# Performance work log

Measured on AMD Instinct MI355X. Metric: run time of the kernel, lower is better.

The kernel has to match this reference:

```python
import jax, jax.numpy as jnp
import numpy as np
import math

B, N, M, C, H = 4, 2048, 2048, 512, 4
D_V = C // H          # 128, used for scale and value head dim
D_QK = 2 * C // H     # 256, q/k head dim due to seq-axis split of the 2*dim qkv output
SCALE = D_V ** -0.5
EPS = 1e-12           # F.normalize eps


def _l2norm(t):
    n = jnp.linalg.norm(t, axis=-1, keepdims=True)
    return t / jnp.maximum(n, EPS)


def setup_inputs() -> dict:
    key = jax.random.key(0)
    k1, k2, k3, k4 = jax.random.split(key, 4)
    x = jax.random.normal(k1, (B, N, C), dtype=jnp.float32)
    context = jax.random.normal(k2, (B, M, C), dtype=jnp.float32)
    W_qkv = jax.random.normal(k3, (2 * C, C), dtype=jnp.float32) * 0.02  # torch Linear weight [out,in]
    W_proj = jax.random.normal(k4, (C, C), dtype=jnp.float32) * 0.02
    radius = jnp.ones((H,), dtype=jnp.float32) * math.sqrt(D_V)
    return {"x": x, "context": context, "W_qkv": W_qkv, "W_proj": W_proj, "radius": radius}


def reference(x, context, W_qkv, W_proj, radius):
    # qkv(cat([x, context], dim=1)) then split along sequence: q from x rows, k from context rows
    q = jnp.einsum('bnc,oc->bno', x, W_qkv)        # [B,N,2C]
    k = jnp.einsum('bmc,oc->bmo', context, W_qkv)  # [B,M,2C]
    q = q.reshape(B, N, H, D_QK).transpose(0, 2, 1, 3)       # [B,H,N,256]
    k = k.reshape(B, M, H, D_QK).transpose(0, 2, 1, 3)       # [B,H,M,256]
    v = context.reshape(B, M, H, D_V).transpose(0, 2, 1, 3)  # [B,H,M,128]
    r = radius[None, :, None, None]
    q = _l2norm(q) * r
    k = _l2norm(k) * r
    attn = jnp.einsum('bhnd,bhmd->bhnm', q, k) * SCALE
    attn = jax.nn.softmax(attn, axis=-1)
    out = jnp.einsum('bhnm,bhmd->bhnd', attn, v)
    out = out.transpose(0, 2, 1, 3).reshape(B, N, C)
    return jnp.einsum('bnc,oc->bno', out, W_proj)
```

## Files before the change

kernel.cpp:

```cpp
#include <hip/hip_runtime.h>
#include <hip/hip_bf16.h>
#include <stdint.h>

#define SCALE_F 0.08838834764831845f
#define LOG2E_F 1.4426950408889634f

typedef __attribute__((ext_vector_type(8))) short short8;
typedef __attribute__((ext_vector_type(4))) float f32x4;
typedef __attribute__((ext_vector_type(16))) float f32x16;
typedef __attribute__((ext_vector_type(2))) unsigned int uint2v;

__device__ __forceinline__ void g2l16(const void* g, void* l) {
  __builtin_amdgcn_global_load_lds(
      (const __attribute__((address_space(1))) void*)g,
      (__attribute__((address_space(3))) void*)l, 16, 0, 0);
}

__device__ __forceinline__ unsigned pkbf(float a, float b) {
  union { __hip_bfloat16 h[2]; unsigned u; } o;
  o.h[0] = __float2bfloat16(a); o.h[1] = __float2bfloat16(b);
  return o.u;
}

__device__ __forceinline__ float fexp2(float x) {
#if __has_builtin(__builtin_amdgcn_exp2f)
  return __builtin_amdgcn_exp2f(x);
#else
  float r; asm("v_exp_f32 %0, %1" : "=v"(r) : "v"(x)); return r;
#endif
}

__global__ __launch_bounds__(256) void convert_all(
    const float* __restrict__ x, const float* __restrict__ wqkv,
    const float* __restrict__ wproj,
    __hip_bfloat16* __restrict__ ab, __hip_bfloat16* __restrict__ wb,
    __hip_bfloat16* __restrict__ wpb)
{
  size_t qi = (size_t)blockIdx.x * 256 + threadIdx.x;
  const float* src; __hip_bfloat16* dst; size_t off;
  if (qi < 1048576)      { src = x;     dst = ab;  off = qi; }
  else if (qi < 1179648) { src = wqkv;  dst = wb;  off = qi - 1048576; }
  else                   { src = wproj; dst = wpb; off = qi - 1179648; }
  float4 v = ((const float4*)src)[off];
  union { __hip_bfloat16 h4[4]; uint2 u; } o;
  o.h4[0] = __float2bfloat16(v.x); o.h4[1] = __float2bfloat16(v.y);
  o.h4[2] = __float2bfloat16(v.z); o.h4[3] = __float2bfloat16(v.w);
  ((uint2*)dst)[off] = o.u;
}

__global__ __launch_bounds__(256) void transpose_v(
    const float* __restrict__ ctx, __hip_bfloat16* __restrict__ vt,
    __hip_bfloat16* __restrict__ abctx)
{
  __shared__ float tile[128][33];
  const int bid = blockIdx.x;
  const int mt = bid & 63;
  const int bh = bid >> 6;
  const int h = bh & 3, b = bh >> 2;
  const int tid = threadIdx.x;
  for (int i = 0; i < 16; ++i) {
    int idx = i * 256 + tid;
    int mm = idx >> 7, d = idx & 127;
    tile[d][mm] = ctx[((size_t)b * 2048 + mt * 32 + mm) * 512 + h * 128 + d];
  }
  __syncthreads();
  for (int i = 0; i < 16; ++i) {
    int idx = i * 256 + tid;
    int d = idx >> 5, mm = idx & 31;
    vt[((size_t)bh * 128 + d) * 2048 + mt * 32 + mm] = __float2bfloat16(tile[d][mm]);
  }
  for (int i = 0; i < 16; ++i) {
    int idx = i * 256 + tid;
    int mm = idx >> 7, d = idx & 127;
    abctx[((size_t)b * 2048 + mt * 32 + mm) * 512 + h * 128 + d] =
        __float2bfloat16(tile[d][mm]);
  }
}

__global__ __launch_bounds__(256) void gemm_qkv(
    const __hip_bfloat16* __restrict__ A,
    const __hip_bfloat16* __restrict__ Bw,
    const float* __restrict__ radius,
    __hip_bfloat16* __restrict__ qn, __hip_bfloat16* __restrict__ kn)
{
  __shared__ __hip_bfloat16 sAB[320 * 32];
  __shared__ float sNorm[4][64];
  __hip_bfloat16* sA = sAB;
  __hip_bfloat16* sB = sAB + 64 * 32;
  const int tid = threadIdx.x;
  const int wave = tid >> 6, lane = tid & 63;
  const int ln = lane & 15, q4 = lane >> 4;
  const int ro = blockIdx.x >> 2;
  const int co = blockIdx.x & 3;
  const __hip_bfloat16* Ab = A + (size_t)ro * 64 * 512;
  const __hip_bfloat16* Bb = Bw + (size_t)co * 256 * 512;
  const int row0 = tid >> 2, p0 = tid & 3;
  f32x4 acc[4][4] = {};
  for (int k0 = 0; k0 < 512; k0 += 32) {
    g2l16(Ab + (size_t)row0 * 512 + k0 + p0 * 8, (char*)sA + tid * 16);
#pragma unroll
    for (int i = 0; i < 4; ++i)
      g2l16(Bb + (size_t)(i * 64 + row0) * 512 + k0 + p0 * 8,
            (char*)sB + (i * 256 + tid) * 16);
    __syncthreads();
    short8 af[4], bfr[4];
#pragma unroll
    for (int mi = 0; mi < 4; ++mi)
      af[mi] = *(const short8*)(sA + (mi * 16 + ln) * 32 + q4 * 8);
#pragma unroll
    for (int ni = 0; ni < 4; ++ni)
      bfr[ni] = *(const short8*)(sB + (wave * 64 + ni * 16 + ln) * 32 + q4 * 8);
#pragma unroll
    for (int mi = 0; mi < 4; ++mi)
#pragma unroll
      for (int ni = 0; ni < 4; ++ni)
        acc[mi][ni] = __builtin_amdgcn_mfma_f32_16x16x32_bf16(af[mi], bfr[ni], acc[mi][ni], 0, 0, 0);
    __syncthreads();
  }
  const float rad = radius[co];
  const int grow0 = ro * 64;
  const bool isq = grow0 < 8192;
  const int rl = isq ? grow0 : grow0 - 8192;
  const float qfac = isq ? rad * rad * SCALE_F * LOG2E_F : 1.0f;
#pragma unroll
  for (int mi = 0; mi < 4; ++mi)
#pragma unroll
    for (int r = 0; r < 4; ++r) {
      float ss = acc[mi][0][r] * acc[mi][0][r] + acc[mi][1][r] * acc[mi][1][r]
               + acc[mi][2][r] * acc[mi][2][r] + acc[mi][3][r] * acc[mi][3][r];
      ss += __shfl_xor(ss, 1); ss += __shfl_xor(ss, 2);
      ss += __shfl_xor(ss, 4); ss += __shfl_xor(ss, 8);
      if (ln == 0) sNorm[wave][mi * 16 + q4 * 4 + r] = ss;
    }
  __syncthreads();
  float scl[4][4];
#pragma unroll
  for (int mi = 0; mi < 4; ++mi)
#pragma unroll
    for (int r = 0; r < 4; ++r) {
      int row = mi * 16 + q4 * 4 + r;
      float tot = sNorm[0][row] + sNorm[1][row] + sNorm[2][row] + sNorm[3][row];
      scl[mi][r] = qfac / fmaxf(sqrtf(tot), 1e-12f);
    }
  __hip_bfloat16* dstT = (isq ? qn : kn) +
      ((size_t)((rl >> 11) * 4 + co) * 2048 + (rl & 2047)) * 256;
  __hip_bfloat16* sE = sAB;
#pragma unroll
  for (int c = 0; c < 2; ++c) {
#pragma unroll
    for (int mi2 = 0; mi2 < 2; ++mi2) {
      int mi = c * 2 + mi2;
#pragma unroll
      for (int r = 0; r < 4; ++r) {
        int lr = mi2 * 16 + q4 * 4 + r;
#pragma unroll
        for (int ni = 0; ni < 4; ++ni)
          sE[lr * 264 + wave * 64 + ni * 16 + ln] =
              __float2bfloat16(acc[mi][ni][r] * scl[mi][r]);
      }
    }
    __syncthreads();
#pragma unroll
    for (int p = 0; p < 4; ++p) {
      int idx = p * 256 + tid;
      int rr = idx >> 5, c8 = idx & 31;
      short8 v = *(const short8*)(sE + rr * 264 + c8 * 8);
      *(short8*)(dstT + (size_t)(c * 32 + rr) * 256 + c8 * 8) = v;
    }
    __syncthreads();
  }
}

__global__ __launch_bounds__(256) void gemm_nt(
    const __hip_bfloat16* __restrict__ A, const __hip_bfloat16* __restrict__ B,
    float* __restrict__ C, int O, int K, int tiles_o)
{
  __shared__ __hip_bfloat16 sA[128 * 32];
  __shared__ __hip_bfloat16 sB[128 * 32];
  const int tid = threadIdx.x;
  const int wave = tid >> 6, lane = tid & 63;
  const int ln = lane & 15, q = lane >> 4;
  const int br = (blockIdx.x / tiles_o) * 128;
  const int bo = (blockIdx.x % tiles_o) * 128;
  const int wr = (wave >> 1) * 64, wc = (wave & 1) * 64;
  const __hip_bfloat16* Ab = A + (size_t)br * K;
  const __hip_bfloat16* Bb = B + (size_t)bo * K;
  const int row0 = tid >> 2, p0 = tid & 3;
  f32x4 acc[4][4] = {};
  for (int k0 = 0; k0 < K; k0 += 32) {
    for (int i = 0; i < 2; ++i) {
      int row = i * 64 + row0;
      g2l16(Ab + (size_t)row * K + k0 + p0 * 8, (char*)sA + (i * 256 + tid) * 16);
      g2l16(Bb + (size_t)row * K + k0 + p0 * 8, (char*)sB + (i * 256 + tid) * 16);
    }
    __syncthreads();
    short8 af[4], bfr[4];
    for (int mi = 0; mi < 4; ++mi)
      af[mi] = *(const short8*)(sA + (wr + mi * 16 + ln) * 32 + q * 8);
    for (int ni = 0; ni < 4; ++ni)
      bfr[ni] = *(const short8*)(sB + (wc + ni * 16 + ln) * 32 + q * 8);
    for (int mi = 0; mi < 4; ++mi)
      for (int ni = 0; ni < 4; ++ni)
        acc[mi][ni] = __builtin_amdgcn_mfma_f32_16x16x32_bf16(af[mi], bfr[ni], acc[mi][ni], 0, 0, 0);
    __syncthreads();
  }
  for (int mi = 0; mi < 4; ++mi)
    for (int ni = 0; ni < 4; ++ni) {
      int rg = br + wr + mi * 16 + q * 4;
      int cg = bo + wc + ni * 16 + ln;
      for (int r = 0; r < 4; ++r)
        C[(size_t)(rg + r) * O + cg] = acc[mi][ni][r];
    }
}

__global__ __launch_bounds__(256, 2) void attn(
    const __hip_bfloat16* __restrict__ qn,
    const __hip_bfloat16* __restrict__ kn,
    const __hip_bfloat16* __restrict__ vt,
    float* __restrict__ Op,
    float* __restrict__ den)
{
  __shared__ __hip_bfloat16 sK[2][32 * 256];
  __shared__ __hip_bfloat16 sV[2][128 * 32];
  const int tid = threadIdx.x, wave = tid >> 6, lane = tid & 63;
  const int m32 = lane & 31, hi = lane >> 5;
  const int i = blockIdx.x;
  const int bh = (i & 7) + 8 * ((i >> 3) & 1);
  const int half = (i >> 4) & 1;
  const int nt = i >> 5;
  const int mbase = half * 1024;
  const __hip_bfloat16* Q = qn + ((size_t)bh * 2048 + nt * 128 + wave * 32) * 256;
  const __hip_bfloat16* Kp = kn + (size_t)bh * 2048 * 256;
  const __hip_bfloat16* Vp = vt + (size_t)bh * 128 * 2048;

  short8 qf[16];
  for (int kk = 0; kk < 16; ++kk)
    qf[kk] = *(const short8*)(Q + m32 * 256 + kk * 16 + hi * 8);

  f32x16 oacc[4];
  for (int v = 0; v < 4; ++v)
    for (int j = 0; j < 16; ++j) oacc[v][j] = 0.f;
  float denom = 0.f;

  for (int t = 0; t < 4; ++t) {
    int D = t * 256 + tid, row = D >> 5, cc = D & 31;
    g2l16(Kp + (size_t)(mbase + row) * 256 + ((cc ^ (row & 7)) << 3),
          (char*)sK[0] + D * 16);
  }
  for (int t = 0; t < 2; ++t) {
    int D = t * 256 + tid, rd = D >> 2, cc = D & 3;
    g2l16(Vp + (size_t)rd * 2048 + mbase + ((cc ^ ((rd >> 1) & 3)) << 3),
          (char*)sV[0] + D * 16);
  }
  __syncthreads();

  for (int it = 0; it < 32; ++it) {
    const int cur = it & 1, nxt = cur ^ 1;
    if (it + 1 < 32) {
      const int m1 = mbase + (it + 1) * 32;
      for (int t = 0; t < 4; ++t) {
        int D = t * 256 + tid, row = D >> 5, cc = D & 31;
        g2l16(Kp + (size_t)(m1 + row) * 256 + ((cc ^ (row & 7)) << 3),
              (char*)sK[nxt] + D * 16);
      }
      for (int t = 0; t < 2; ++t) {
        int D = t * 256 + tid, rd = D >> 2, cc = D & 3;
        g2l16(Vp + (size_t)rd * 2048 + m1 + ((cc ^ ((rd >> 1) & 3)) << 3),
              (char*)sV[nxt] + D * 16);
      }
    }
    const __hip_bfloat16* sKc = sK[cur];
    f32x16 sa, sb;
    for (int j = 0; j < 16; ++j) { sa[j] = 0.f; sb[j] = 0.f; }
#pragma unroll
    for (int kk = 0; kk < 8; ++kk) {
      int ca = kk * 2 + hi, cb = (kk + 8) * 2 + hi;
      short8 kfa = *(const short8*)(sKc + m32 * 256 + ((ca ^ (m32 & 7)) << 3));
      short8 kfb = *(const short8*)(sKc + m32 * 256 + ((cb ^ (m32 & 7)) << 3));
      sa = __builtin_amdgcn_mfma_f32_32x32x16_bf16(kfa, qf[kk], sa, 0, 0, 0);
      sb = __builtin_amdgcn_mfma_f32_32x32x16_bf16(kfb, qf[kk + 8], sb, 0, 0, 0);
    }
    union { unsigned u[4]; short8 s; } ua, ub;
    {
      float e0, e1, e2, e3;
      unsigned u0, u1, u2, u3;
      e0 = fexp2(sa[0] + sb[0]); e1 = fexp2(sa[1] + sb[1]);
      e2 = fexp2(sa[2] + sb[2]); e3 = fexp2(sa[3] + sb[3]);
      denom += (e0 + e1) + (e2 + e3);
      u0 = pkbf(e0, e1); u1 = pkbf(e2, e3);
      e0 = fexp2(sa[4] + sb[4]); e1 = fexp2(sa[5] + sb[5]);
      e2 = fexp2(sa[6] + sb[6]); e3 = fexp2(sa[7] + sb[7]);
      denom += (e0 + e1) + (e2 + e3);
      u2 = pkbf(e0, e1); u3 = pkbf(e2, e3);
      uint2v s0 = __builtin_amdgcn_permlane32_swap(u0, u2, false, false);
      uint2v s1 = __builtin_amdgcn_permlane32_swap(u1, u3, false, false);
      ua.u[0] = s0.x; ua.u[1] = s1.x; ua.u[2] = s0.y; ua.u[3] = s1.y;
      e0 = fexp2(sa[8] + sb[8]);   e1 = fexp2(sa[9] + sb[9]);
      e2 = fexp2(sa[10] + sb[10]); e3 = fexp2(sa[11] + sb[11]);
      denom += (e0 + e1) + (e2 + e3);
      u0 = pkbf(e0, e1); u1 = pkbf(e2, e3);
      e0 = fexp2(sa[12] + sb[12]); e1 = fexp2(sa[13] + sb[13]);
      e2 = fexp2(sa[14] + sb[14]); e3 = fexp2(sa[15] + sb[15]);
      denom += (e0 + e1) + (e2 + e3);
      u2 = pkbf(e0, e1); u3 = pkbf(e2, e3);
      uint2v s2 = __builtin_amdgcn_permlane32_swap(u0, u2, false, false);
      uint2v s3 = __builtin_amdgcn_permlane32_swap(u1, u3, false, false);
      ub.u[0] = s2.x; ub.u[1] = s3.x; ub.u[2] = s2.y; ub.u[3] = s3.y;
    }
    const __hip_bfloat16* sVc = sV[cur];
#pragma unroll
    for (int kc = 0; kc < 2; ++kc) {
      short8 pf = kc ? ub.s : ua.s;
#pragma unroll
      for (int vi = 0; vi < 4; ++vi) {
        int rd = vi * 32 + m32;
        int c = kc * 2 + hi;
        short8 vf = *(const short8*)(sVc + rd * 32 + ((c ^ ((rd >> 1) & 3)) << 3));
        oacc[vi] = __builtin_amdgcn_mfma_f32_32x32x16_bf16(vf, pf, oacc[vi], 0, 0, 0);
      }
    }
    __syncthreads();
  }

  float dfull = denom + __shfl_xor(denom, 32);
  float* Opb = Op + (size_t)(half * 16 + bh) * 2048 * 128;
  float* denb = den + (size_t)(half * 16 + bh) * 2048;
  const int rbase = nt * 128 + wave * 32;
  if (hi == 0) denb[rbase + m32] = dfull;
  float* sc_ = (float*)(&sK[0][0]) + wave * 1056;
#pragma unroll
  for (int vi = 0; vi < 4; ++vi) {
#pragma unroll
    for (int reg = 0; reg < 16; ++reg) {
      int dL = (reg & 3) + 8 * (reg >> 2) + 4 * hi;
      sc_[m32 * 33 + dL] = oacc[vi][reg];
    }
    asm volatile("s_waitcnt lgkmcnt(0)" ::: "memory");
#pragma unroll
    for (int qq = 0; qq < 16; ++qq) {
      int qr = qq * 2 + hi;
      Opb[(size_t)(rbase + qr) * 128 + vi * 32 + m32] = sc_[qr * 33 + m32];
    }
    asm volatile("s_waitcnt lgkmcnt(0)" ::: "memory");
  }
}

__global__ __launch_bounds__(256) void combine(
    const float* __restrict__ Op, const float* __restrict__ den,
    __hip_bfloat16* __restrict__ ob)
{
  int qi = blockIdx.x * 256 + threadIdx.x;
  int r = qi >> 5;
  int dq = qi & 31;
  int bh = r >> 11, n = r & 2047, b = bh >> 2, h = bh & 3;
  float4 o0 = ((const float4*)Op)[qi];
  float4 o1 = ((const float4*)(Op + 4194304))[qi];
  float inv = 1.0f / (den[r] + den[32768 + r]);
  union { __hip_bfloat16 h4[4]; uint2 u; } o;
  o.h4[0] = __float2bfloat16((o0.x + o1.x) * inv);
  o.h4[1] = __float2bfloat16((o0.y + o1.y) * inv);
  o.h4[2] = __float2bfloat16((o0.z + o1.z) * inv);
  o.h4[3] = __float2bfloat16((o0.w + o1.w) * inv);
  *(uint2*)&ob[((size_t)b * 2048 + n) * 512 + h * 128 + dq * 4] = o.u;
}

extern "C" void kernel_launch(void* const* d_in, const int* in_sizes, int n_in,
                              void* d_out, int out_size, void* d_ws, size_t ws_size,
                              hipStream_t stream) {
  const float* x      = (const float*)d_in[0];
  const float* ctx    = (const float*)d_in[1];
  const float* wqkv   = (const float*)d_in[2];
  const float* wproj  = (const float*)d_in[3];
  const float* radius = (const float*)d_in[4];
  char* ws = (char*)d_ws;
  __hip_bfloat16* ab  = (__hip_bfloat16*)(ws);
  __hip_bfloat16* wb  = (__hip_bfloat16*)(ws + 16777216);
  __hip_bfloat16* wpb = (__hip_bfloat16*)(ws + 17825792);
  float*          Op  = (float*)(ws + 18350080);
  float*          den = (float*)(ws + 18350080 + 33554432);
  __hip_bfloat16* qn  = (__hip_bfloat16*)(ws + 85458944);
  __hip_bfloat16* kn  = (__hip_bfloat16*)(ws + 102236160);
  __hip_bfloat16* vt  = (__hip_bfloat16*)(ws + 119013376);
  __hip_bfloat16* ob  = (__hip_bfloat16*)(ws + 127401984);
  float* out = (float*)d_out;

  convert_all<<<4864, 256, 0, stream>>>(x, wqkv, wproj, ab, wb, wpb);
  transpose_v<<<1024, 256, 0, stream>>>(ctx, vt, ab + 4194304);
  gemm_qkv<<<1024, 256, 0, stream>>>(ab, wb, radius, qn, kn);
  attn<<<512, 256, 0, stream>>>(qn, kn, vt, Op, den);
  combine<<<4096, 256, 0, stream>>>(Op, den, ob);
  gemm_nt<<<256, 256, 0, stream>>>(ob, wpb, out, 512, 512, 4);
}
```

Baseline: 214.3 us.

## Software-pipeline QK and softmax-PV across KV tiles with triple buffering

The attention loop is restructured so each iteration issues the QK^T MFMAs for the next KV tile before the exp/pack and PV MFMAs of the current tile. A third LDS buffer holds the extra tile in flight, and the waits become explicit vmcnt waits plus barriers. This lets exp and permlane work overlap with matrix ops, at the cost of more registers for a second score set and more LDS per block. The output projection GEMM is specialized to 128x64 tiles with 512 blocks for better CU coverage.

Measured after the change: 242.8 us. +13.3%, slower.

```diff
diff --git a/kernel.cpp b/kernel.cpp
--- a/kernel.cpp
+++ b/kernel.cpp
@@ -171,46 +171,128 @@
   }
 }
 
-__global__ __launch_bounds__(256) void gemm_nt(
-    const __hip_bfloat16* __restrict__ A, const __hip_bfloat16* __restrict__ B,
-    float* __restrict__ C, int O, int K, int tiles_o)
+__global__ __launch_bounds__(256) void gemm_proj(
+    const __hip_bfloat16* __restrict__ A,
+    const __hip_bfloat16* __restrict__ B,
+    float* __restrict__ C)
 {
   __shared__ __hip_bfloat16 sA[128 * 32];
-  __shared__ __hip_bfloat16 sB[128 * 32];
+  __shared__ __hip_bfloat16 sB[64 * 32];
   const int tid = threadIdx.x;
   const int wave = tid >> 6, lane = tid & 63;
   const int ln = lane & 15, q = lane >> 4;
-  const int br = (blockIdx.x / tiles_o) * 128;
-  const int bo = (blockIdx.x % tiles_o) * 128;
-  const int wr = (wave >> 1) * 64, wc = (wave & 1) * 64;
-  const __hip_bfloat16* Ab = A + (size_t)br * K;
-  const __hip_bfloat16* Bb = B + (size_t)bo * K;
+  const int br = (blockIdx.x >> 3) * 128;
+  const int bo = (blockIdx.x & 7) * 64;
+  const int wr = (wave >> 1) * 64, wc = (wave & 1) * 32;
   const int row0 = tid >> 2, p0 = tid & 3;
-  f32x4 acc[4][4] = {};
-  for (int k0 = 0; k0 < K; k0 += 32) {
-    for (int i = 0; i < 2; ++i) {
-      int row = i * 64 + row0;
-      g2l16(Ab + (size_t)row * K + k0 + p0 * 8, (char*)sA + (i * 256 + tid) * 16);
-      g2l16(Bb + (size_t)row * K + k0 + p0 * 8, (char*)sB + (i * 256 + tid) * 16);
-    }
-    __syncthreads();
-    short8 af[4], bfr[4];
+  f32x4 acc[4][2] = {};
+  for (int k0 = 0; k0 < 512; k0 += 32) {
+    g2l16(A + (size_t)(br + row0) * 512 + k0 + p0 * 8, (char*)sA + tid * 16);
+    g2l16(A + (size_t)(br + 64 + row0) * 512 + k0 + p0 * 8,
+          (char*)sA + (256 + tid) * 16);
+    g2l16(B + (size_t)(bo + row0) * 512 + k0 + p0 * 8, (char*)sB + tid * 16);
+    __syncthreads();
+    short8 af[4], bfr[2];
+#pragma unroll
     for (int mi = 0; mi < 4; ++mi)
       af[mi] = *(const short8*)(sA + (wr + mi * 16 + ln) * 32 + q * 8);
-    for (int ni = 0; ni < 4; ++ni)
+#pragma unroll
+    for (int ni = 0; ni < 2; ++ni)
       bfr[ni] = *(const short8*)(sB + (wc + ni * 16 + ln) * 32 + q * 8);
+#pragma unroll
     for (int mi = 0; mi < 4; ++mi)
-      for (int ni = 0; ni < 4; ++ni)
+#pragma unroll
+      for (int ni = 0; ni < 2; ++ni)
         acc[mi][ni] = __builtin_amdgcn_mfma_f32_16x16x32_bf16(af[mi], bfr[ni], acc[mi][ni], 0, 0, 0);
     __syncthreads();
   }
+#pragma unroll
   for (int mi = 0; mi < 4; ++mi)
-    for (int ni = 0; ni < 4; ++ni) {
+#pragma unroll
+    for (int ni = 0; ni < 2; ++ni) {
       int rg = br + wr + mi * 16 + q * 4;
       int cg = bo + wc + ni * 16 + ln;
+#pragma unroll
       for (int r = 0; r < 4; ++r)
-        C[(size_t)(rg + r) * O + cg] = acc[mi][ni][r];
-    }
+        C[(size_t)(rg + r) * 512 + cg] = acc[mi][ni][r];
+    }
+}
+
+__device__ __forceinline__ void stage_kv(
+    const __hip_bfloat16* __restrict__ Kp, const __hip_bfloat16* __restrict__ Vp,
+    int mrow, __hip_bfloat16* dK, __hip_bfloat16* dV, int tid)
+{
+#pragma unroll
+  for (int t = 0; t < 4; ++t) {
+    int D = t * 256 + tid, row = D >> 5, cc = D & 31;
+    g2l16(Kp + (size_t)(mrow + row) * 256 + ((cc ^ (row & 7)) << 3),
+          (char*)dK + D * 16);
+  }
+#pragma unroll
+  for (int t = 0; t < 2; ++t) {
+    int D = t * 256 + tid, rd = D >> 2, cc = D & 3;
+    g2l16(Vp + (size_t)rd * 2048 + mrow + ((cc ^ ((rd >> 1) & 3)) << 3),
+          (char*)dV + D * 16);
+  }
+}
+
+__device__ __forceinline__ void qk_step(
+    const __hip_bfloat16* __restrict__ sKc, const short8* qf,
+    int m32, int hi, f32x16& sa, f32x16& sb)
+{
+  for (int j = 0; j < 16; ++j) { sa[j] = 0.f; sb[j] = 0.f; }
+#pragma unroll
+  for (int kk = 0; kk < 8; ++kk) {
+    int ca = kk * 2 + hi, cb = (kk + 8) * 2 + hi;
+    short8 kfa = *(const short8*)(sKc + m32 * 256 + ((ca ^ (m32 & 7)) << 3));
+    short8 kfb = *(const short8*)(sKc + m32 * 256 + ((cb ^ (m32 & 7)) << 3));
+    sa = __builtin_amdgcn_mfma_f32_32x32x16_bf16(kfa, qf[kk], sa, 0, 0, 0);
+    sb = __builtin_amdgcn_mfma_f32_32x32x16_bf16(kfb, qf[kk + 8], sb, 0, 0, 0);
+  }
+}
+
+__device__ __forceinline__ void smpv_step(
+    const f32x16& sa, const f32x16& sb, const __hip_bfloat16* __restrict__ sVc,
+    int m32, int hi, f32x16* oacc, float& denom)
+{
+  union { unsigned u[4]; short8 s; } ua, ub;
+  {
+    float e0, e1, e2, e3;
+    unsigned u0, u1, u2, u3;
+    e0 = fexp2(sa[0] + sb[0]); e1 = fexp2(sa[1] + sb[1]);
+    e2 = fexp2(sa[2] + sb[2]); e3 = fexp2(sa[3] + sb[3]);
+    denom += (e0 + e1) + (e2 + e3);
+    u0 = pkbf(e0, e1); u1 = pkbf(e2, e3);
+    e0 = fexp2(sa[4] + sb[4]); e1 = fexp2(sa[5] + sb[5]);
+    e2 = fexp2(sa[6] + sb[6]); e3 = fexp2(sa[7] + sb[7]);
+    denom += (e0 + e1) + (e2 + e3);
+    u2 = pkbf(e0, e1); u3 = pkbf(e2, e3);
+    uint2v s0 = __builtin_amdgcn_permlane32_swap(u0, u2, false, false);
+    uint2v s1 = __builtin_amdgcn_permlane32_swap(u1, u3, false, false);
+    ua.u[0] = s0.x; ua.u[1] = s1.x; ua.u[2] = s0.y; ua.u[3] = s1.y;
+    e0 = fexp2(sa[8] + sb[8]);   e1 = fexp2(sa[9] + sb[9]);
+    e2 = fexp2(sa[10] + sb[10]); e3 = fexp2(sa[11] + sb[11]);
+    denom += (e0 + e1) + (e2 + e3);
+    u0 = pkbf(e0, e1); u1 = pkbf(e2, e3);
+    e0 = fexp2(sa[12] + sb[12]); e1 = fexp2(sa[13] + sb[13]);
+    e2 = fexp2(sa[14] + sb[14]); e3 = fexp2(sa[15] + sb[15]);
+    denom += (e0 + e1) + (e2 + e3);
+    u2 = pkbf(e0, e1); u3 = pkbf(e2, e3);
+    uint2v s2 = __builtin_amdgcn_permlane32_swap(u0, u2, false, false);
+    uint2v s3 = __builtin_amdgcn_permlane32_swap(u1, u3, false, false);
+    ub.u[0] = s2.x; ub.u[1] = s3.x; ub.u[2] = s2.y; ub.u[3] = s3.y;
+  }
+#pragma unroll
+  for (int kc = 0; kc < 2; ++kc) {
+    short8 pf = kc ? ub.s : ua.s;
+#pragma unroll
+    for (int vi = 0; vi < 4; ++vi) {
+      int rd = vi * 32 + m32;
+      int c = kc * 2 + hi;
+      short8 vf = *(const short8*)(sVc + rd * 32 + ((c ^ ((rd >> 1) & 3)) << 3));
+      oacc[vi] = __builtin_amdgcn_mfma_f32_32x32x16_bf16(vf, pf, oacc[vi], 0, 0, 0);
+    }
+  }
 }
 
 __global__ __launch_bounds__(256, 2) void attn(
@@ -220,8 +302,8 @@
     float* __restrict__ Op,
     float* __restrict__ den)
 {
-  __shared__ __hip_bfloat16 sK[2][32 * 256];
-  __shared__ __hip_bfloat16 sV[2][128 * 32];
+  __shared__ __hip_bfloat16 sK[3][32 * 256];
+  __shared__ __hip_bfloat16 sV[3][128 * 32];
   const int tid = threadIdx.x, wave = tid >> 6, lane = tid & 63;
   const int m32 = lane & 31, hi = lane >> 5;
   const int i = blockIdx.x;
@@ -242,84 +324,30 @@
     for (int j = 0; j < 16; ++j) oacc[v][j] = 0.f;
   float denom = 0.f;
 
-  for (int t = 0; t < 4; ++t) {
-    int D = t * 256 + tid, row = D >> 5, cc = D & 31;
-    g2l16(Kp + (size_t)(mbase + row) * 256 + ((cc ^ (row & 7)) << 3),
-          (char*)sK[0] + D * 16);
-  }
-  for (int t = 0; t < 2; ++t) {
-    int D = t * 256 + tid, rd = D >> 2, cc = D & 3;
-    g2l16(Vp + (size_t)rd * 2048 + mbase + ((cc ^ ((rd >> 1) & 3)) << 3),
-          (char*)sV[0] + D * 16);
-  }
-  __syncthreads();
-
-  for (int it = 0; it < 32; ++it) {
-    const int cur = it & 1, nxt = cur ^ 1;
-    if (it + 1 < 32) {
-      const int m1 = mbase + (it + 1) * 32;
-      for (int t = 0; t < 4; ++t) {
-        int D = t * 256 + tid, row = D >> 5, cc = D & 31;
-        g2l16(Kp + (size_t)(m1 + row) * 256 + ((cc ^ (row & 7)) << 3),
-              (char*)sK[nxt] + D * 16);
-      }
-      for (int t = 0; t < 2; ++t) {
-        int D = t * 256 + tid, rd = D >> 2, cc = D & 3;
-        g2l16(Vp + (size_t)rd * 2048 + m1 + ((cc ^ ((rd >> 1) & 3)) << 3),
-              (char*)sV[nxt] + D * 16);
-      }
-    }
-    const __hip_bfloat16* sKc = sK[cur];
-    f32x16 sa, sb;
-    for (int j = 0; j < 16; ++j) { sa[j] = 0.f; sb[j] = 0.f; }
-#pragma unroll
-    for (int kk = 0; kk < 8; ++kk) {
-      int ca = kk * 2 + hi, cb = (kk + 8) * 2 + hi;
-      short8 kfa = *(const short8*)(sKc + m32 * 256 + ((ca ^ (m32 & 7)) << 3));
-      short8 kfb = *(const short8*)(sKc + m32 * 256 + ((cb ^ (m32 & 7)) << 3));
-      sa = __builtin_amdgcn_mfma_f32_32x32x16_bf16(kfa, qf[kk], sa, 0, 0, 0);
-      sb = __builtin_amdgcn_mfma_f32_32x32x16_bf16(kfb, qf[kk + 8], sb, 0, 0, 0);
-    }
-    union { unsigned u[4]; short8 s; } ua, ub;
-    {
-      float e0, e1, e2, e3;
-      unsigned u0, u1, u2, u3;
-      e0 = fexp2(sa[0] + sb[0]); e1 = fexp2(sa[1] + sb[1]);
-      e2 = fexp2(sa[2] + sb[2]); e3 = fexp2(sa[3] + sb[3]);
-      denom += (e0 + e1) + (e2 + e3);
-      u0 = pkbf(e0, e1); u1 = pkbf(e2, e3);
-      e0 = fexp2(sa[4] + sb[4]); e1 = fexp2(sa[5] + sb[5]);
-      e2 = fexp2(sa[6] + sb[6]); e3 = fexp2(sa[7] + sb[7]);
-      denom += (e0 + e1) + (e2 + e3);
-      u2 = pkbf(e0, e1); u3 = pkbf(e2, e3);
-      uint2v s0 = __builtin_amdgcn_permlane32_swap(u0, u2, false, false);
-      uint2v s1 = __builtin_amdgcn_permlane32_swap(u1, u3, false, false);
-      ua.u[0] = s0.x; ua.u[1] = s1.x; ua.u[2] = s0.y; ua.u[3] = s1.y;
-      e0 = fexp2(sa[8] + sb[8]);   e1 = fexp2(sa[9] + sb[9]);
-      e2 = fexp2(sa[10] + sb[10]); e3 = fexp2(sa[11] + sb[11]);
-      denom += (e0 + e1) + (e2 + e3);
-      u0 = pkbf(e0, e1); u1 = pkbf(e2, e3);
-      e0 = fexp2(sa[12] + sb[12]); e1 = fexp2(sa[13] + sb[13]);
-      e2 = fexp2(sa[14] + sb[14]); e3 = fexp2(sa[15] + sb[15]);
-      denom += (e0 + e1) + (e2 + e3);
-      u2 = pkbf(e0, e1); u3 = pkbf(e2, e3);
-      uint2v s2 = __builtin_amdgcn_permlane32_swap(u0, u2, false, false);
-      uint2v s3 = __builtin_amdgcn_permlane32_swap(u1, u3, false, false);
-      ub.u[0] = s2.x; ub.u[1] = s3.x; ub.u[2] = s2.y; ub.u[3] = s3.y;
-    }
-    const __hip_bfloat16* sVc = sV[cur];
-#pragma unroll
-    for (int kc = 0; kc < 2; ++kc) {
-      short8 pf = kc ? ub.s : ua.s;
-#pragma unroll
-      for (int vi = 0; vi < 4; ++vi) {
-        int rd = vi * 32 + m32;
-        int c = kc * 2 + hi;
-        short8 vf = *(const short8*)(sVc + rd * 32 + ((c ^ ((rd >> 1) & 3)) << 3));
-        oacc[vi] = __builtin_amdgcn_mfma_f32_32x32x16_bf16(vf, pf, oacc[vi], 0, 0, 0);
-      }
-    }
-    __syncthreads();
+  int p0 = 0, p1 = 1, p2 = 2;
+
+  stage_kv(Kp, Vp, mbase,      sK[0], sV[0], tid);
+  stage_kv(Kp, Vp, mbase + 32, sK[1], sV[1], tid);
+  asm volatile("s_waitcnt vmcnt(0)" ::: "memory");
+  __builtin_amdgcn_s_barrier();
+  f32x16 saE, sbE, saO, sbO;
+  qk_step(sK[0], qf, m32, hi, saE, sbE);
+
+  for (int it = 0; it < 32; it += 2) {
+    asm volatile("s_waitcnt vmcnt(0)" ::: "memory");
+    __builtin_amdgcn_s_barrier();
+    if (it + 2 < 32)
+      stage_kv(Kp, Vp, mbase + (it + 2) * 32, sK[p2], sV[p2], tid);
+    qk_step(sK[p1], qf, m32, hi, saO, sbO);
+    smpv_step(saE, sbE, sV[p0], m32, hi, oacc, denom);
+    asm volatile("s_waitcnt vmcnt(0)" ::: "memory");
+    __builtin_amdgcn_s_barrier();
+    if (it + 3 < 32)
+      stage_kv(Kp, Vp, mbase + (it + 3) * 32, sK[p0], sV[p0], tid);
+    if (it + 2 < 32)
+      qk_step(sK[p2], qf, m32, hi, saE, sbE);
+    smpv_step(saO, sbO, sV[p1], m32, hi, oacc, denom);
+    int t = p0; p0 = p2; p2 = p1; p1 = t;
   }
 
   float dfull = denom + __shfl_xor(denom, 32);
@@ -389,5 +417,5 @@
   gemm_qkv<<<1024, 256, 0, stream>>>(ab, wb, radius, qn, kn);
   attn<<<512, 256, 0, stream>>>(qn, kn, vt, Op, den);
   combine<<<4096, 256, 0, stream>>>(Op, den, ob);
-  gemm_nt<<<256, 256, 0, stream>>>(ob, wpb, out, 512, 512, 4);
-}
+  gemm_proj<<<512, 256, 0, stream>>>(ob, wpb, out);
+}
```
